# Performance work log

Hardware: AMD Instinct MI355X
Metric: run time of the kernel (lower is better)

Reference implementation:

```python
import jax, jax.numpy as jnp
import numpy as np

D_IN, D_OUT, N_TOK = 4096, 4096, 8192

def _binarize(w):
    # sign with straight-through estimator (sign(0) treated as sign output of jnp.sign)
    return w + jax.lax.stop_gradient(jnp.sign(w) - w)

def setup_inputs() -> dict:
    key = jax.random.key(0)
    k1, k2, k3, k4, k5 = jax.random.split(key, 5)
    x = jax.random.normal(k1, (N_TOK, D_IN), dtype=jnp.float32)
    W1 = jax.random.normal(k2, (D_OUT, D_IN), dtype=jnp.float32)
    W2 = jax.random.normal(k3, (D_OUT, D_IN), dtype=jnp.float32)
    b1 = jax.random.normal(k4, (D_OUT,), dtype=jnp.float32)
    b2 = jax.random.normal(k5, (D_OUT,), dtype=jnp.float32)
    return {"x": x, "W1": W1, "W2": W2, "b1": b1, "b2": b2}

def reference(x, W1, W2, b1, b2):
    # BinaryLinear: F.linear(x, sign(W), b); TernaryLinear = binary1(x) - binary2(x)
    out1 = x @ _binarize(W1).T + b1
    out2 = x @ _binarize(W2).T + b2
    return out1 - out2
```

## Files before the change

kernel.cpp:

```cpp
#include <hip/hip_runtime.h>


#define DIM_K 4096
#define DIM_N 4096
#define DIM_M 8192

typedef _Float16 f16x8 __attribute__((ext_vector_type(8)));
typedef _Float16 f16x4 __attribute__((ext_vector_type(4)));
typedef float    f32x4 __attribute__((ext_vector_type(4)));


__global__ void cvt_x_kernel(const float4* __restrict__ x, f16x4* __restrict__ xh) {
    const int i = blockIdx.x * blockDim.x + threadIdx.x;
    const float4 v = x[i];
    f16x4 h;
    h[0] = (_Float16)v.x; h[1] = (_Float16)v.y;
    h[2] = (_Float16)v.z; h[3] = (_Float16)v.w;
    xh[i] = h;
}

__device__ __forceinline__ float signdiff(float a, float b) {
    const float sa = (float)((a > 0.f) - (a < 0.f));
    const float sb = (float)((b > 0.f) - (b < 0.f));
    return sa - sb;
}

__global__ void cvt_w_kernel(const float4* __restrict__ w1,
                             const float4* __restrict__ w2,
                             f16x4* __restrict__ wh) {
    const int i = blockIdx.x * blockDim.x + threadIdx.x;
    const float4 a = w1[i];
    const float4 b = w2[i];
    f16x4 h;
    h[0] = (_Float16)signdiff(a.x, b.x);
    h[1] = (_Float16)signdiff(a.y, b.y);
    h[2] = (_Float16)signdiff(a.z, b.z);
    h[3] = (_Float16)signdiff(a.w, b.w);
    wh[i] = h;
}

__global__ void cvt_b_kernel(const float* __restrict__ b1,
                             const float* __restrict__ b2,
                             float* __restrict__ bd) {
    const int i = blockIdx.x * blockDim.x + threadIdx.x;
    bd[i] = b1[i] - b2[i];
}


__global__ __launch_bounds__(256, 2) void ternary_gemm(
    const _Float16* __restrict__ Xh, const _Float16* __restrict__ Wh,
    const float* __restrict__ bd, float* __restrict__ C) {
    __shared__ __align__(16) char smem[32768];

    const int tid  = threadIdx.x;
    const int wave = tid >> 6;
    const int lane = tid & 63;
    const int wm = wave >> 1, wn = wave & 1;
    const int q = lane >> 4, r = lane & 15;

    const int lrow   = lane >> 3;
    const int lchunk = lane & 7;
    const int gchunk = lchunk ^ lrow;
    const int srow   = wave * 8 + lrow;

    const int bRowM = blockIdx.y * 128;
    const int bColN = blockIdx.x * 128;

    const char* aPtr = (const char*)Xh + (size_t)(bRowM + srow) * (DIM_K * 2) + gchunk * 16;
    const char* bPtr = (const char*)Wh + (size_t)(bColN + srow) * (DIM_K * 2) + gchunk * 16;

    char* const ldsA = smem + wave * 1024;
    char* const ldsB = smem + 16384 + wave * 1024;

    const char* const aRd = smem + (wm * 64 + r) * 128;
    const char* const bRd = smem + 16384 + (wn * 64 + r) * 128;
    const int sc0 = ((0 * 4 + q) ^ (r & 7)) * 16;
    const int sc1 = ((1 * 4 + q) ^ (r & 7)) * 16;

    f32x4 acc[4][4] = {};

    for (int kt = 0; kt < DIM_K; kt += 64) {
        __syncthreads();
#pragma unroll
        for (int i = 0; i < 4; ++i) {
            __builtin_amdgcn_global_load_lds(
                (const __attribute__((address_space(1))) void*)(aPtr + (size_t)i * 262144),
                (__attribute__((address_space(3))) void*)(ldsA + i * 4096), 16, 0, 0);
            __builtin_amdgcn_global_load_lds(
                (const __attribute__((address_space(1))) void*)(bPtr + (size_t)i * 262144),
                (__attribute__((address_space(3))) void*)(ldsB + i * 4096), 16, 0, 0);
        }
        __syncthreads();

#pragma unroll
        for (int kk = 0; kk < 2; ++kk) {
            const int sc = kk ? sc1 : sc0;
            f16x8 af[4], bf[4];
#pragma unroll
            for (int t = 0; t < 4; ++t) {
                af[t] = *(const f16x8*)(aRd + t * 2048 + sc);
                bf[t] = *(const f16x8*)(bRd + t * 2048 + sc);
            }
#pragma unroll
            for (int im = 0; im < 4; ++im)
#pragma unroll
                for (int in = 0; in < 4; ++in)
                    acc[im][in] = __builtin_amdgcn_mfma_f32_16x16x32_f16(
                        af[im], bf[in], acc[im][in], 0, 0, 0);
        }
        aPtr += 128;
        bPtr += 128;
    }

    const int col0 = bColN + wn * 64 + r;
    const int row0 = bRowM + wm * 64 + q * 4;
    float bias[4];
#pragma unroll
    for (int in = 0; in < 4; ++in) bias[in] = bd[col0 + in * 16];
#pragma unroll
    for (int im = 0; im < 4; ++im) {
#pragma unroll
        for (int in = 0; in < 4; ++in) {
            const f32x4 v = acc[im][in];
            const int col = col0 + in * 16;
            const size_t base = (size_t)(row0 + im * 16) * DIM_N + col;
#pragma unroll
            for (int j = 0; j < 4; ++j)
                C[base + (size_t)j * DIM_N] = v[j] + bias[in];
        }
    }
}


extern "C" void kernel_launch(void* const* d_in, const int* in_sizes, int n_in,
                              void* d_out, int out_size, void* d_ws, size_t ws_size,
                              hipStream_t stream) {
    const float* x  = (const float*)d_in[0];
    const float* W1 = (const float*)d_in[1];
    const float* W2 = (const float*)d_in[2];
    const float* b1 = (const float*)d_in[3];
    const float* b2 = (const float*)d_in[4];
    float* out = (float*)d_out;

    _Float16* Xh = (_Float16*)d_ws;
    _Float16* Wh = (_Float16*)((char*)d_ws + (size_t)67108864);
    float*    bd = (float*)((char*)d_ws + (size_t)67108864 + 33554432);
    (void)ws_size; (void)in_sizes; (void)n_in; (void)out_size;

    cvt_x_kernel<<<32768, 256, 0, stream>>>((const float4*)x, (f16x4*)Xh);
    cvt_w_kernel<<<16384, 256, 0, stream>>>((const float4*)W1, (const float4*)W2, (f16x4*)Wh);
    cvt_b_kernel<<<16, 256, 0, stream>>>(b1, b2, bd);

    ternary_gemm<<<dim3(32, 64), 256, 0, stream>>>(Xh, Wh, bd, out);
}
```

Before: 553.7 us.

## Rewrite GEMM with 256x256 tiles, double-buffered LDS pipeline, fused conversion kernel

```diff
diff --git a/kernel.cpp b/kernel.cpp
--- a/kernel.cpp
+++ b/kernel.cpp
@@ -6,18 +6,8 @@
 #define DIM_M 8192
 
 typedef _Float16 f16x8 __attribute__((ext_vector_type(8)));
-typedef _Float16 f16x4 __attribute__((ext_vector_type(4)));
 typedef float    f32x4 __attribute__((ext_vector_type(4)));
 
-
-__global__ void cvt_x_kernel(const float4* __restrict__ x, f16x4* __restrict__ xh) {
-    const int i = blockIdx.x * blockDim.x + threadIdx.x;
-    const float4 v = x[i];
-    f16x4 h;
-    h[0] = (_Float16)v.x; h[1] = (_Float16)v.y;
-    h[2] = (_Float16)v.z; h[3] = (_Float16)v.w;
-    xh[i] = h;
-}
 
 __device__ __forceinline__ float signdiff(float a, float b) {
     const float sa = (float)((a > 0.f) - (a < 0.f));
@@ -25,110 +15,232 @@
     return sa - sb;
 }
 
-__global__ void cvt_w_kernel(const float4* __restrict__ w1,
-                             const float4* __restrict__ w2,
-                             f16x4* __restrict__ wh) {
-    const int i = blockIdx.x * blockDim.x + threadIdx.x;
-    const float4 a = w1[i];
-    const float4 b = w2[i];
-    f16x4 h;
-    h[0] = (_Float16)signdiff(a.x, b.x);
-    h[1] = (_Float16)signdiff(a.y, b.y);
-    h[2] = (_Float16)signdiff(a.z, b.z);
-    h[3] = (_Float16)signdiff(a.w, b.w);
-    wh[i] = h;
-}
-
-__global__ void cvt_b_kernel(const float* __restrict__ b1,
-                             const float* __restrict__ b2,
-                             float* __restrict__ bd) {
-    const int i = blockIdx.x * blockDim.x + threadIdx.x;
-    bd[i] = b1[i] - b2[i];
-}
-
-
-__global__ __launch_bounds__(256, 2) void ternary_gemm(
+__global__ void cvt_fused(const float4* __restrict__ x,
+                          const float4* __restrict__ w1,
+                          const float4* __restrict__ w2,
+                          f16x8* __restrict__ xh,
+                          f16x8* __restrict__ wh) {
+    const int XU = DIM_M * DIM_K / 8;
+    const int TU = XU + DIM_N * DIM_K / 8;
+    const int stride = gridDim.x * blockDim.x;
+    for (int u = blockIdx.x * blockDim.x + threadIdx.x; u < TU; u += stride) {
+        if (u < XU) {
+            const float4 a = x[2 * u], b = x[2 * u + 1];
+            f16x8 h;
+            h[0] = (_Float16)a.x; h[1] = (_Float16)a.y;
+            h[2] = (_Float16)a.z; h[3] = (_Float16)a.w;
+            h[4] = (_Float16)b.x; h[5] = (_Float16)b.y;
+            h[6] = (_Float16)b.z; h[7] = (_Float16)b.w;
+            xh[u] = h;
+        } else {
+            const int v = u - XU;
+            const float4 a1 = w1[2 * v], b1 = w1[2 * v + 1];
+            const float4 a2 = w2[2 * v], b2 = w2[2 * v + 1];
+            f16x8 h;
+            h[0] = (_Float16)signdiff(a1.x, a2.x);
+            h[1] = (_Float16)signdiff(a1.y, a2.y);
+            h[2] = (_Float16)signdiff(a1.z, a2.z);
+            h[3] = (_Float16)signdiff(a1.w, a2.w);
+            h[4] = (_Float16)signdiff(b1.x, b2.x);
+            h[5] = (_Float16)signdiff(b1.y, b2.y);
+            h[6] = (_Float16)signdiff(b1.z, b2.z);
+            h[7] = (_Float16)signdiff(b1.w, b2.w);
+            wh[v] = h;
+        }
+    }
+}
+
+
+__global__ __launch_bounds__(512, 2) void ternary_gemm(
     const _Float16* __restrict__ Xh, const _Float16* __restrict__ Wh,
-    const float* __restrict__ bd, float* __restrict__ C) {
-    __shared__ __align__(16) char smem[32768];
+    const float* __restrict__ B1, const float* __restrict__ B2,
+    float* __restrict__ C) {
+    __shared__ __align__(16) char smem[131072];
 
     const int tid  = threadIdx.x;
     const int wave = tid >> 6;
     const int lane = tid & 63;
-    const int wm = wave >> 1, wn = wave & 1;
-    const int q = lane >> 4, r = lane & 15;
-
-    const int lrow   = lane >> 3;
-    const int lchunk = lane & 7;
-    const int gchunk = lchunk ^ lrow;
-    const int srow   = wave * 8 + lrow;
-
-    const int bRowM = blockIdx.y * 128;
-    const int bColN = blockIdx.x * 128;
-
-    const char* aPtr = (const char*)Xh + (size_t)(bRowM + srow) * (DIM_K * 2) + gchunk * 16;
-    const char* bPtr = (const char*)Wh + (size_t)(bColN + srow) * (DIM_K * 2) + gchunk * 16;
-
-    char* const ldsA = smem + wave * 1024;
-    char* const ldsB = smem + 16384 + wave * 1024;
-
-    const char* const aRd = smem + (wm * 64 + r) * 128;
-    const char* const bRd = smem + 16384 + (wn * 64 + r) * 128;
-    const int sc0 = ((0 * 4 + q) ^ (r & 7)) * 16;
-    const int sc1 = ((1 * 4 + q) ^ (r & 7)) * 16;
-
-    f32x4 acc[4][4] = {};
-
-    for (int kt = 0; kt < DIM_K; kt += 64) {
-        __syncthreads();
-#pragma unroll
-        for (int i = 0; i < 4; ++i) {
-            __builtin_amdgcn_global_load_lds(
-                (const __attribute__((address_space(1))) void*)(aPtr + (size_t)i * 262144),
-                (__attribute__((address_space(3))) void*)(ldsA + i * 4096), 16, 0, 0);
-            __builtin_amdgcn_global_load_lds(
-                (const __attribute__((address_space(1))) void*)(bPtr + (size_t)i * 262144),
-                (__attribute__((address_space(3))) void*)(ldsB + i * 4096), 16, 0, 0);
-        }
-        __syncthreads();
-
-#pragma unroll
-        for (int kk = 0; kk < 2; ++kk) {
-            const int sc = kk ? sc1 : sc0;
-            f16x8 af[4], bf[4];
-#pragma unroll
-            for (int t = 0; t < 4; ++t) {
-                af[t] = *(const f16x8*)(aRd + t * 2048 + sc);
-                bf[t] = *(const f16x8*)(bRd + t * 2048 + sc);
+    const int wm = wave >> 2;
+    const int wn = wave & 3;
+    const int q  = lane >> 4;
+    const int r  = lane & 15;
+
+    const int bid = blockIdx.x;
+    const int id  = (bid & 7) * 64 + (bid >> 3);
+    const int bRowM = (id >> 4) * 256;
+    const int bColN = (id & 15) * 256;
+
+    const int srow   = tid >> 3;
+    const int gchunk = (tid & 7) ^ (srow & 7);
+    const char* aSrc = (const char*)Xh + (size_t)(bRowM + srow) * (DIM_K * 2) + gchunk * 16;
+    const char* bSrc = (const char*)Wh + (size_t)(bColN + srow) * (DIM_K * 2) + gchunk * 16;
+    char* const ldsBase = smem;
+    const int waveOff = wave * 1024;
+
+#define STAGE_A(bufsel, h, dk) do {                                                             \
+    _Pragma("unroll")                                                                           \
+    for (int i_ = 0; i_ < 2; ++i_)                                                              \
+        __builtin_amdgcn_global_load_lds(                                                       \
+            (const __attribute__((address_space(1))) void*)(                                    \
+                aSrc + (size_t)((h) * 128 + i_ * 64) * (DIM_K * 2) + (dk) * 128),               \
+            (__attribute__((address_space(3))) void*)(                                          \
+                ldsBase + (bufsel) * 32768 + ((h) * 128 + i_ * 64) * 128 + waveOff),            \
+            16, 0, 0);                                                                          \
+} while (0)
+#define STAGE_B(bufsel, h, dk) do {                                                             \
+    _Pragma("unroll")                                                                           \
+    for (int i_ = 0; i_ < 2; ++i_)                                                              \
+        __builtin_amdgcn_global_load_lds(                                                       \
+            (const __attribute__((address_space(1))) void*)(                                    \
+                bSrc + (size_t)((h) * 128 + i_ * 64) * (DIM_K * 2) + (dk) * 128),               \
+            (__attribute__((address_space(3))) void*)(                                          \
+                ldsBase + 65536 + (bufsel) * 32768 + ((h) * 128 + i_ * 64) * 128 + waveOff),    \
+            16, 0, 0);                                                                          \
+} while (0)
+
+    const int swz = r & 7;
+    char* const aRd = smem + (wm * 64 + r) * 128;
+    char* const bRd = smem + 65536 + (wn * 32 + r) * 128;
+    const int ck0 = ((0 * 4 + q) ^ swz) * 16;
+    const int ck1 = ((1 * 4 + q) ^ swz) * 16;
+
+    f32x4 acc[2][2][4][2] = {};
+    f16x8 af[4][2], bf0[2][2], bf1[2][2];
+
+    STAGE_A(0, 0, 0);
+    STAGE_B(0, 0, 0);
+    STAGE_A(0, 1, 0);
+    STAGE_B(0, 1, 0);
+    STAGE_A(1, 0, 1);
+    STAGE_B(1, 0, 1);
+    asm volatile("s_waitcnt vmcnt(4)" ::: "memory");
+    __builtin_amdgcn_s_barrier();
+    __builtin_amdgcn_sched_barrier(0);
+
+    for (int kt = 0; kt < 64; ++kt) {
+        const int cur = kt & 1, nxt = cur ^ 1;
+        const char* const aC = aRd + cur * 32768;
+        const char* const bC = bRd + cur * 32768;
+
+#pragma unroll
+        for (int im = 0; im < 4; ++im) {
+            af[im][0] = *(const f16x8*)(aC + im * 2048 + ck0);
+            af[im][1] = *(const f16x8*)(aC + im * 2048 + ck1);
+        }
+#pragma unroll
+        for (int in = 0; in < 2; ++in) {
+            bf0[in][0] = *(const f16x8*)(bC + in * 2048 + ck0);
+            bf0[in][1] = *(const f16x8*)(bC + in * 2048 + ck1);
+        }
+        if (kt < 63) STAGE_A(nxt, 1, 1);
+        __builtin_amdgcn_s_barrier();
+        asm volatile("s_waitcnt lgkmcnt(0)" ::: "memory");
+        __builtin_amdgcn_sched_barrier(0);
+        __builtin_amdgcn_s_setprio(1);
+#pragma unroll
+        for (int im = 0; im < 4; ++im)
+#pragma unroll
+            for (int in = 0; in < 2; ++in)
+#pragma unroll
+                for (int kk = 0; kk < 2; ++kk)
+                    acc[0][0][im][in] = __builtin_amdgcn_mfma_f32_16x16x32_f16(
+                        af[im][kk], bf0[in][kk], acc[0][0][im][in], 0, 0, 0);
+        __builtin_amdgcn_s_setprio(0);
+        __builtin_amdgcn_sched_barrier(0);
+        __builtin_amdgcn_s_barrier();
+        __builtin_amdgcn_sched_barrier(0);
+
+#pragma unroll
+        for (int in = 0; in < 2; ++in) {
+            bf1[in][0] = *(const f16x8*)(bC + 16384 + in * 2048 + ck0);
+            bf1[in][1] = *(const f16x8*)(bC + 16384 + in * 2048 + ck1);
+        }
+        if (kt < 63) STAGE_B(nxt, 1, 1);
+        __builtin_amdgcn_s_barrier();
+        asm volatile("s_waitcnt lgkmcnt(0)" ::: "memory");
+        __builtin_amdgcn_sched_barrier(0);
+        __builtin_amdgcn_s_setprio(1);
+#pragma unroll
+        for (int im = 0; im < 4; ++im)
+#pragma unroll
+            for (int in = 0; in < 2; ++in)
+#pragma unroll
+                for (int kk = 0; kk < 2; ++kk)
+                    acc[0][1][im][in] = __builtin_amdgcn_mfma_f32_16x16x32_f16(
+                        af[im][kk], bf1[in][kk], acc[0][1][im][in], 0, 0, 0);
+        __builtin_amdgcn_s_setprio(0);
+        __builtin_amdgcn_sched_barrier(0);
+        __builtin_amdgcn_s_barrier();
+        __builtin_amdgcn_sched_barrier(0);
+
+#pragma unroll
+        for (int im = 0; im < 4; ++im) {
+            af[im][0] = *(const f16x8*)(aC + 16384 + im * 2048 + ck0);
+            af[im][1] = *(const f16x8*)(aC + 16384 + im * 2048 + ck1);
+        }
+        if (kt < 62) STAGE_A(cur, 0, 2);
+        __builtin_amdgcn_s_barrier();
+        asm volatile("s_waitcnt lgkmcnt(0)" ::: "memory");
+        __builtin_amdgcn_sched_barrier(0);
+        __builtin_amdgcn_s_setprio(1);
+#pragma unroll
+        for (int im = 0; im < 4; ++im)
+#pragma unroll
+            for (int in = 0; in < 2; ++in)
+#pragma unroll
+                for (int kk = 0; kk < 2; ++kk)
+                    acc[1][0][im][in] = __builtin_amdgcn_mfma_f32_16x16x32_f16(
+                        af[im][kk], bf0[in][kk], acc[1][0][im][in], 0, 0, 0);
+        __builtin_amdgcn_s_setprio(0);
+        __builtin_amdgcn_sched_barrier(0);
+        __builtin_amdgcn_s_barrier();
+        __builtin_amdgcn_sched_barrier(0);
+
+        if (kt < 62) STAGE_B(cur, 0, 2);
+        __builtin_amdgcn_s_barrier();
+        __builtin_amdgcn_s_setprio(1);
+#pragma unroll
+        for (int im = 0; im < 4; ++im)
+#pragma unroll
+            for (int in = 0; in < 2; ++in)
+#pragma unroll
+                for (int kk = 0; kk < 2; ++kk)
+                    acc[1][1][im][in] = __builtin_amdgcn_mfma_f32_16x16x32_f16(
+                        af[im][kk], bf1[in][kk], acc[1][1][im][in], 0, 0, 0);
+        __builtin_amdgcn_s_setprio(0);
+        if (kt < 62) {
+            asm volatile("s_waitcnt vmcnt(4)" ::: "memory");
+        } else if (kt == 62) {
+            asm volatile("s_waitcnt vmcnt(0)" ::: "memory");
+        }
+        __builtin_amdgcn_s_barrier();
+        __builtin_amdgcn_sched_barrier(0);
+
+        aSrc += 128;
+        bSrc += 128;
+    }
+
+#pragma unroll
+    for (int nh = 0; nh < 2; ++nh) {
+#pragma unroll
+        for (int in = 0; in < 2; ++in) {
+            const int col = bColN + nh * 128 + wn * 32 + in * 16 + r;
+            const float bia = B1[col] - B2[col];
+#pragma unroll
+            for (int mh = 0; mh < 2; ++mh) {
+#pragma unroll
+                for (int im = 0; im < 4; ++im) {
+                    const int row0 = bRowM + mh * 128 + wm * 64 + im * 16 + q * 4;
+                    const f32x4 v = acc[mh][nh][im][in];
+#pragma unroll
+                    for (int j = 0; j < 4; ++j)
+                        C[(size_t)(row0 + j) * DIM_N + col] = v[j] + bia;
+                }
             }
-#pragma unroll
-            for (int im = 0; im < 4; ++im)
-#pragma unroll
-                for (int in = 0; in < 4; ++in)
-                    acc[im][in] = __builtin_amdgcn_mfma_f32_16x16x32_f16(
-                        af[im], bf[in], acc[im][in], 0, 0, 0);
-        }
-        aPtr += 128;
-        bPtr += 128;
+        }
     }
-
-    const int col0 = bColN + wn * 64 + r;
-    const int row0 = bRowM + wm * 64 + q * 4;
-    float bias[4];
-#pragma unroll
-    for (int in = 0; in < 4; ++in) bias[in] = bd[col0 + in * 16];
-#pragma unroll
-    for (int im = 0; im < 4; ++im) {
-#pragma unroll
-        for (int in = 0; in < 4; ++in) {
-            const f32x4 v = acc[im][in];
-            const int col = col0 + in * 16;
-            const size_t base = (size_t)(row0 + im * 16) * DIM_N + col;
-#pragma unroll
-            for (int j = 0; j < 4; ++j)
-                C[base + (size_t)j * DIM_N] = v[j] + bias[in];
-        }
-    }
+#undef STAGE_A
+#undef STAGE_B
 }
 
 
@@ -144,12 +256,10 @@
 
     _Float16* Xh = (_Float16*)d_ws;
     _Float16* Wh = (_Float16*)((char*)d_ws + (size_t)67108864);
-    float*    bd = (float*)((char*)d_ws + (size_t)67108864 + 33554432);
     (void)ws_size; (void)in_sizes; (void)n_in; (void)out_size;
 
-    cvt_x_kernel<<<32768, 256, 0, stream>>>((const float4*)x, (f16x4*)Xh);
-    cvt_w_kernel<<<16384, 256, 0, stream>>>((const float4*)W1, (const float4*)W2, (f16x4*)Wh);
-    cvt_b_kernel<<<16, 256, 0, stream>>>(b1, b2, bd);
-
-    ternary_gemm<<<dim3(32, 64), 256, 0, stream>>>(Xh, Wh, bd, out);
-}
+    cvt_fused<<<2048, 256, 0, stream>>>((const float4*)x, (const float4*)W1,
+                                        (const float4*)W2, (f16x8*)Xh, (f16x8*)Wh);
+
+    ternary_gemm<<<512, 512, 0, stream>>>(Xh, Wh, b1, b2, out);
+}
```

After: 527.4 us. 4.8% less time.
